# Optimization experiments

Measured on AMD Instinct MI355X. Metric: run time of the kernel, lower is better.

## Reference

```python
import jax, jax.numpy as jnp
import numpy as np

SPATIAL_SHAPES = np.array([[100, 150], [50, 75], [25, 38], [13, 19]], dtype=np.int64)


def setup_inputs() -> dict:
    key = jax.random.key(0)
    k1, k2, k3 = jax.random.split(key, 3)
    B, heads, d = 1, 8, 32
    L, P = SPATIAL_SHAPES.shape[0], 4
    n_tokens = int(SPATIAL_SHAPES.prod(axis=1).sum())  # 19947
    Q = n_tokens
    value = jax.random.normal(k1, (B, n_tokens, heads, d), dtype=jnp.float32)
    sampling_locations = jax.random.uniform(k2, (B, Q, heads, L, P, 2), dtype=jnp.float32)
    aw = jax.random.uniform(k3, (B, Q, heads, L, P), dtype=jnp.float32)
    # normalize like the real module (softmax over L*P); keeps magnitudes realistic
    attention_weights = aw / aw.sum(axis=(-2, -1), keepdims=True)
    level_start = np.concatenate([[0], np.cumsum(SPATIAL_SHAPES.prod(axis=1))[:-1]]).astype(np.int64)
    return {
        'value': value,
        'value_spatial_shapes': jnp.asarray(SPATIAL_SHAPES),
        'value_level_start_index': jnp.asarray(level_start),
        'sampling_locations': sampling_locations,
        'attention_weights': attention_weights,
        'im2col_step': 64,
    }


def _sample_level(v, loc, Hh, Ww):
    """Bilinear grid_sample (align_corners=False, zero padding).
    v:   [B, heads, Hh*Ww, D]
    loc: [B, Q, heads, P, 2] normalized in [0,1]
    returns [B, heads, Q, P, D]
    """
    B, Q, heads, P, _ = loc.shape
    D = v.shape[-1]
    # grid = 2*loc - 1; pixel coord = (grid+1)*size/2 - 0.5  ==  loc*size - 0.5
    x = loc[..., 0] * Ww - 0.5
    y = loc[..., 1] * Hh - 0.5
    x0f = jnp.floor(x)
    y0f = jnp.floor(y)
    wx1 = x - x0f
    wy1 = y - y0f
    x0 = x0f.astype(jnp.int32)
    y0 = y0f.astype(jnp.int32)

    def gather(xi, yi):
        valid = ((xi >= 0) & (xi < Ww) & (yi >= 0) & (yi < Hh)).astype(v.dtype)
        idx = jnp.clip(yi, 0, Hh - 1) * Ww + jnp.clip(xi, 0, Ww - 1)  # [B,Q,heads,P]
        idx_t = idx.transpose(0, 2, 1, 3).reshape(B, heads, Q * P, 1)
        g = jnp.take_along_axis(v, idx_t, axis=2)  # [B,heads,Q*P,D]
        g = g.reshape(B, heads, Q, P, D)
        return g, valid.transpose(0, 2, 1, 3)[..., None]

    g00, m00 = gather(x0, y0)
    g01, m01 = gather(x0 + 1, y0)
    g10, m10 = gather(x0, y0 + 1)
    g11, m11 = gather(x0 + 1, y0 + 1)
    wx1t = wx1.transpose(0, 2, 1, 3)[..., None]
    wy1t = wy1.transpose(0, 2, 1, 3)[..., None]
    wx0t = 1.0 - wx1t
    wy0t = 1.0 - wy1t
    return (g00 * m00 * (wx0t * wy0t) + g01 * m01 * (wx1t * wy0t)
            + g10 * m10 * (wx0t * wy1t) + g11 * m11 * (wx1t * wy1t))


def msda_forward(value, spatial_shapes_np, sampling_locations, attention_weights):
    B, n_tokens, heads, D = value.shape
    Q = sampling_locations.shape[1]
    areas = [int(h) * int(w) for h, w in spatial_shapes_np]
    # value per level as [B, heads, H*W, D]
    v_bhnd = value.transpose(0, 2, 1, 3)  # [B, heads, N, D]
    out = jnp.zeros((B, Q, heads, D), dtype=value.dtype)
    start = 0
    for lvl, (Hh, Ww) in enumerate(spatial_shapes_np):
        Hh, Ww = int(Hh), int(Ww)
        v_l = jax.lax.slice_in_dim(v_bhnd, start, start + Hh * Ww, axis=2)
        loc_l = sampling_locations[:, :, :, lvl]  # [B,Q,heads,P,2]
        sampled = _sample_level(v_l, loc_l, Hh, Ww)  # [B,heads,Q,P,D]
        aw_l = attention_weights[:, :, :, lvl]  # [B,Q,heads,P]
        out = out + jnp.einsum('bhqpd,bqhp->bqhd', sampled, aw_l)
        start += Hh * Ww
    return out.reshape(B, Q, heads * D)


def reference(value, value_spatial_shapes, value_level_start_index, sampling_locations, attention_weights, im2col_step):
    spatial_shapes_np = np.asarray(jax.device_get(value_spatial_shapes))
    return msda_forward(value, spatial_shapes_np, sampling_locations, attention_weights)
```

## Files before the change

kernel.cpp:

```cpp
#include <hip/hip_runtime.h>


typedef float    f32x4 __attribute__((ext_vector_type(4)));
typedef float    f32x8 __attribute__((ext_vector_type(8)));
typedef _Float16 f16x8 __attribute__((ext_vector_type(8)));

constexpr int HEADS = 8;
constexpr int DCH   = 32;
constexpr int NSP   = 16;
constexpr int NQ    = 19947;
constexpr int QPB   = 32;
constexpr int HSTR  = NQ * DCH;
constexpr int NVAL  = NQ * HEADS * DCH;

__global__ __launch_bounds__(256)
void cvt_kernel(const float* __restrict__ value, _Float16* __restrict__ ws)
{
    const int h = blockIdx.x & 7;
    const int i = (blockIdx.x >> 3) * 256 + threadIdx.x;
    if (i >= NQ * 4) return;
    const int c8  = i & 3;
    const int tok = i >> 2;
    const float* src = value + (size_t)tok * 256 + h * 32 + c8 * 8;
    const f32x4 a = __builtin_nontemporal_load((const f32x4*)src);
    const f32x4 b = __builtin_nontemporal_load((const f32x4*)(src + 4));
    const f32x8 v = {a.x, a.y, a.z, a.w, b.x, b.y, b.z, b.w};
    *(f16x8*)(ws + (size_t)h * HSTR + (size_t)tok * 32 + c8 * 8) =
        __builtin_convertvector(v, f16x8);
}

template <bool F16>
__global__ __launch_bounds__(256)
void msda_fwd_kernel(const void* __restrict__ valuev,
                     const float* __restrict__ loc,
                     const float* __restrict__ attw,
                     float* __restrict__ out)
{
    __shared__ float s_loc[QPB][33];
    __shared__ float s_aw [QPB][17];

    const int h    = blockIdx.x & 7;
    const int qblk = blockIdx.x >> 3;
    const int q0   = qblk * QPB;
    const int t    = threadIdx.x;

    {
        const int sub = t >> 3, j = t & 7;
        const int q = q0 + sub;
        if (q < NQ) {
            const f32x4 v = __builtin_nontemporal_load(
                (const f32x4*)(loc + ((size_t)(q * HEADS + h)) * (NSP * 2) + j * 4));
            const int l = j >> 1;
            const float fW = (l == 0) ? 150.f : (l == 1) ? 75.f : (l == 2) ? 38.f : 19.f;
            const float fH = (l == 0) ? 100.f : (l == 1) ? 50.f : (l == 2) ? 25.f : 13.f;
            s_loc[sub][j * 4 + 0] = v.x * fW - 0.5f;
            s_loc[sub][j * 4 + 1] = v.y * fH - 0.5f;
            s_loc[sub][j * 4 + 2] = v.z * fW - 0.5f;
            s_loc[sub][j * 4 + 3] = v.w * fH - 0.5f;
        }
    }
    if (t < 128) {
        const int sub = t >> 2, j = t & 3;
        const int q = q0 + sub;
        if (q < NQ) {
            const f32x4 w = __builtin_nontemporal_load(
                (const f32x4*)(attw + ((size_t)(q * HEADS + h)) * NSP + j * 4));
            s_aw[sub][j * 4 + 0] = w.x;
            s_aw[sub][j * 4 + 1] = w.y;
            s_aw[sub][j * 4 + 2] = w.z;
            s_aw[sub][j * 4 + 3] = w.w;
        }
    }
    __syncthreads();

    const int sub  = t >> 3;
    const int jj   = t & 3;
    const int half = (t >> 2) & 1;
    const int q    = q0 + sub;
    if (q >= NQ) return;

    const _Float16* vf16 = (const _Float16*)valuev + (size_t)h * HSTR + jj * 8;
    const float*    vf32 = (const float*)valuev + h * DCH + jj * 8;

    auto meta = [&](int sp, f32x4& c, int& i00, int& i01, int& i10, int& i11) {
        const int l = sp >> 2;
        const int W = (l == 0) ? 150 : (l == 1) ? 75 : (l == 2) ? 38 : 19;
        const int H = (l == 0) ? 100 : (l == 1) ? 50 : (l == 2) ? 25 : 13;
        const int S = (l == 0) ? 0 : (l == 1) ? 15000 : (l == 2) ? 18750 : 19700;
        const float x  = s_loc[sub][sp * 2 + 0];
        const float y  = s_loc[sub][sp * 2 + 1];
        const float aw = s_aw[sub][sp];
        const float x0f = floorf(x);
        const float y0f = floorf(y);
        const float wx1 = x - x0f;
        const float wy1 = y - y0f;
        const float wx0 = 1.f - wx1;
        const float wy0 = 1.f - wy1;
        const int x0 = (int)x0f, y0 = (int)y0f;
        const int x1 = x0 + 1,   y1 = y0 + 1;
        const float wx0m = ((unsigned)x0 < (unsigned)W) ? wx0 : 0.f;
        const float wx1m = ((unsigned)x1 < (unsigned)W) ? wx1 : 0.f;
        const float wy0m = ((unsigned)y0 < (unsigned)H) ? aw * wy0 : 0.f;
        const float wy1m = ((unsigned)y1 < (unsigned)H) ? aw * wy1 : 0.f;
        c.x = wy0m * wx0m;
        c.y = wy0m * wx1m;
        c.z = wy1m * wx0m;
        c.w = wy1m * wx1m;
        const int cx0 = max(x0, 0), cx1 = min(x1, W - 1);
        const int cy0 = max(y0, 0), cy1 = min(y1, H - 1);
        const int r0 = S + cy0 * W;
        const int r1 = S + cy1 * W;
        i00 = r0 + cx0; i01 = r0 + cx1; i10 = r1 + cx0; i11 = r1 + cx1;
    };

    f32x8 acc = {0.f, 0.f, 0.f, 0.f, 0.f, 0.f, 0.f, 0.f};
    const int sp0 = half * 8;

#pragma unroll
    for (int u = 0; u < 8; ++u) {
        const int sp = sp0 + u;
        f32x4 c;
        int i00, i01, i10, i11;
        meta(sp, c, i00, i01, i10, i11);

        if constexpr (F16) {
            const f16x8 g00 = *(const f16x8*)(vf16 + (size_t)i00 * 32);
            const f16x8 g01 = *(const f16x8*)(vf16 + (size_t)i01 * 32);
            const f16x8 g10 = *(const f16x8*)(vf16 + (size_t)i10 * 32);
            const f16x8 g11 = *(const f16x8*)(vf16 + (size_t)i11 * 32);
#pragma unroll
            for (int k = 0; k < 8; ++k) {
                acc[k] += c.x * (float)g00[k];
                acc[k] += c.y * (float)g01[k];
                acc[k] += c.z * (float)g10[k];
                acc[k] += c.w * (float)g11[k];
            }
        } else {
            const f32x4 a0 = *(const f32x4*)(vf32 + ((size_t)i00 << 8));
            const f32x4 a1 = *(const f32x4*)(vf32 + ((size_t)i00 << 8) + 4);
            const f32x4 b0 = *(const f32x4*)(vf32 + ((size_t)i01 << 8));
            const f32x4 b1 = *(const f32x4*)(vf32 + ((size_t)i01 << 8) + 4);
            const f32x4 c0 = *(const f32x4*)(vf32 + ((size_t)i10 << 8));
            const f32x4 c1 = *(const f32x4*)(vf32 + ((size_t)i10 << 8) + 4);
            const f32x4 d0 = *(const f32x4*)(vf32 + ((size_t)i11 << 8));
            const f32x4 d1 = *(const f32x4*)(vf32 + ((size_t)i11 << 8) + 4);
#pragma unroll
            for (int k = 0; k < 4; ++k) {
                acc[k]     += c.x * a0[k] + c.y * b0[k] + c.z * c0[k] + c.w * d0[k];
                acc[k + 4] += c.x * a1[k] + c.y * b1[k] + c.z * c1[k] + c.w * d1[k];
            }
        }
    }

#pragma unroll
    for (int k = 0; k < 8; ++k) acc[k] += __shfl_xor(acc[k], 4);

    float* op = out + (size_t)(q * HEADS + h) * DCH + jj * 8 + half * 4;
    const f32x4 part = half ? f32x4{acc[4], acc[5], acc[6], acc[7]}
                            : f32x4{acc[0], acc[1], acc[2], acc[3]};
    __builtin_nontemporal_store(part, (f32x4*)op);
}

extern "C" void kernel_launch(void* const* d_in, const int* in_sizes, int n_in,
                              void* d_out, int out_size, void* d_ws, size_t ws_size,
                              hipStream_t stream) {
    const float* value = (const float*)d_in[0];
    const float* loc   = (const float*)d_in[3];
    const float* attw  = (const float*)d_in[4];
    float* out = (float*)d_out;

    const int qblocks = (NQ + QPB - 1) / QPB;
    const int grid = qblocks * HEADS;

    const size_t f16_bytes = (size_t)NVAL * sizeof(_Float16);
    if (ws_size >= f16_bytes) {
        _Float16* ws = (_Float16*)d_ws;
        const int cgrid = ((NQ * 4 + 255) / 256) * HEADS;
        cvt_kernel<<<cgrid, 256, 0, stream>>>(value, ws);
        msda_fwd_kernel<true><<<grid, 256, 0, stream>>>(ws, loc, attw, out);
    } else {
        msda_fwd_kernel<false><<<grid, 256, 0, stream>>>(value, loc, attw, out);
    }
}
```

Baseline: 55.05 us.

## Store horizontally adjacent value pairs in fp16 workspace to halve bilinear gathers

The conversion kernel now writes each token's fp16 channels interleaved with those of the next token (x+1). Each bilinear sample then needs only two 32-byte row loads instead of four 16-byte corner loads, and lanes split between the left and right neighbour. The x-edge clamp case folds both weights onto the left element. The cost is a doubled workspace write plus a larger gather footprint, fewer queries per block, and an extra shuffle reduction. The new path runs only when the workspace is large enough, which it must be for the new branch to be taken.

```diff
diff --git a/kernel.cpp b/kernel.cpp
--- a/kernel.cpp
+++ b/kernel.cpp
@@ -9,9 +9,32 @@
 constexpr int DCH   = 32;
 constexpr int NSP   = 16;
 constexpr int NQ    = 19947;
-constexpr int QPB   = 32;
-constexpr int HSTR  = NQ * DCH;
+constexpr int HSTR1 = NQ * DCH;
+constexpr int HSTR2 = NQ * 64;
 constexpr int NVAL  = NQ * HEADS * DCH;
+
+__global__ __launch_bounds__(256)
+void cvt_pair_kernel(const float* __restrict__ value, _Float16* __restrict__ ws)
+{
+    const int h = blockIdx.x & 7;
+    const int i = (blockIdx.x >> 3) * 256 + threadIdx.x;
+    if (i >= NQ * 4) return;
+    const int jj = i & 3;
+    const int t  = i >> 2;
+    const float* src = value + (size_t)t * 256 + h * 32 + jj * 8;
+    const f32x4 a = __builtin_nontemporal_load((const f32x4*)src);
+    const f32x4 b = __builtin_nontemporal_load((const f32x4*)(src + 4));
+    const f32x8 v = {a.x, a.y, a.z, a.w, b.x, b.y, b.z, b.w};
+    const f16x8 o = __builtin_convertvector(v, f16x8);
+    _Float16* base = ws + (size_t)h * HSTR2;
+    *(f16x8*)(base + (size_t)t * 64 + jj * 16) = o;
+    if (t > 0)
+        *(f16x8*)(base + (size_t)(t - 1) * 64 + jj * 16 + 8) = o;
+    if (t == NQ - 1) {
+        const f16x8 z = {};
+        *(f16x8*)(base + (size_t)t * 64 + jj * 16 + 8) = z;
+    }
+}
 
 __global__ __launch_bounds__(256)
 void cvt_kernel(const float* __restrict__ value, _Float16* __restrict__ ws)
@@ -25,8 +48,127 @@
     const f32x4 a = __builtin_nontemporal_load((const f32x4*)src);
     const f32x4 b = __builtin_nontemporal_load((const f32x4*)(src + 4));
     const f32x8 v = {a.x, a.y, a.z, a.w, b.x, b.y, b.z, b.w};
-    *(f16x8*)(ws + (size_t)h * HSTR + (size_t)tok * 32 + c8 * 8) =
+    *(f16x8*)(ws + (size_t)h * HSTR1 + (size_t)tok * 32 + c8 * 8) =
         __builtin_convertvector(v, f16x8);
+}
+
+__global__ __launch_bounds__(256)
+void msda_pair_kernel(const _Float16* __restrict__ ws,
+                      const float* __restrict__ loc,
+                      const float* __restrict__ attw,
+                      float* __restrict__ out)
+{
+    constexpr int QPB = 16;
+    __shared__ float s_loc[QPB][33];
+    __shared__ float s_aw [QPB][17];
+
+    const int h    = blockIdx.x & 7;
+    const int qblk = blockIdx.x >> 3;
+    const int q0   = qblk * QPB;
+    const int t    = threadIdx.x;
+
+    if (t < 128) {
+        const int sub = t >> 3, j = t & 7;
+        const int q = q0 + sub;
+        if (q < NQ) {
+            const f32x4 v = __builtin_nontemporal_load(
+                (const f32x4*)(loc + ((size_t)(q * HEADS + h)) * (NSP * 2) + j * 4));
+            const int l = j >> 1;
+            const float fW = (l == 0) ? 150.f : (l == 1) ? 75.f : (l == 2) ? 38.f : 19.f;
+            const float fH = (l == 0) ? 100.f : (l == 1) ? 50.f : (l == 2) ? 25.f : 13.f;
+            s_loc[sub][j * 4 + 0] = v.x * fW - 0.5f;
+            s_loc[sub][j * 4 + 1] = v.y * fH - 0.5f;
+            s_loc[sub][j * 4 + 2] = v.z * fW - 0.5f;
+            s_loc[sub][j * 4 + 3] = v.w * fH - 0.5f;
+        }
+    } else if (t < 192) {
+        const int u = t - 128;
+        const int sub = u >> 2, j = u & 3;
+        const int q = q0 + sub;
+        if (q < NQ) {
+            const f32x4 w = __builtin_nontemporal_load(
+                (const f32x4*)(attw + ((size_t)(q * HEADS + h)) * NSP + j * 4));
+            s_aw[sub][j * 4 + 0] = w.x;
+            s_aw[sub][j * 4 + 1] = w.y;
+            s_aw[sub][j * 4 + 2] = w.z;
+            s_aw[sub][j * 4 + 3] = w.w;
+        }
+    }
+    __syncthreads();
+
+    const int sub  = t >> 4;
+    const int ll   = t & 15;
+    const int half = ll >> 3;
+    const int g    = (ll >> 1) & 3;
+    const int s    = ll & 1;
+    const int q    = q0 + sub;
+    if (q >= NQ) return;
+
+    const _Float16* vf = ws + (size_t)h * HSTR2 + g * 16 + s * 8;
+
+    f32x8 acc = {0.f, 0.f, 0.f, 0.f, 0.f, 0.f, 0.f, 0.f};
+    const int sp0 = half * 8;
+
+#pragma unroll
+    for (int u = 0; u < 8; ++u) {
+        const int sp = sp0 + u;
+        const int l  = sp >> 2;
+        const int W = (l == 0) ? 150 : (l == 1) ? 75 : (l == 2) ? 38 : 19;
+        const int H = (l == 0) ? 100 : (l == 1) ? 50 : (l == 2) ? 25 : 13;
+        const int S = (l == 0) ? 0 : (l == 1) ? 15000 : (l == 2) ? 18750 : 19700;
+
+        const float x  = s_loc[sub][sp * 2 + 0];
+        const float y  = s_loc[sub][sp * 2 + 1];
+        const float aw = s_aw[sub][sp];
+
+        const float x0f = floorf(x);
+        const float y0f = floorf(y);
+        const float wx1 = x - x0f;
+        const float wy1 = y - y0f;
+        const float wx0 = 1.f - wx1;
+        const float wy0 = 1.f - wy1;
+        const int x0 = (int)x0f, y0 = (int)y0f;
+        const int x1 = x0 + 1,   y1 = y0 + 1;
+
+        const float wx0m = ((unsigned)x0 < (unsigned)W) ? wx0 : 0.f;
+        const float wx1m = ((unsigned)x1 < (unsigned)W) ? wx1 : 0.f;
+        const float wy0m = ((unsigned)y0 < (unsigned)H) ? aw * wy0 : 0.f;
+        const float wy1m = ((unsigned)y1 < (unsigned)H) ? aw * wy1 : 0.f;
+        const float c00 = wy0m * wx0m;
+        const float c01 = wy0m * wx1m;
+        const float c10 = wy1m * wx0m;
+        const float c11 = wy1m * wx1m;
+
+        const int cx0 = max(x0, 0), cx1 = min(x1, W - 1);
+        const int cy0 = max(y0, 0), cy1 = min(y1, H - 1);
+        const bool xi = cx1 > cx0;
+
+        const float fA = s ? (xi ? c01 : 0.f) : (xi ? c00 : c00 + c01);
+        const float fB = s ? (xi ? c11 : 0.f) : (xi ? c10 : c10 + c11);
+
+        const int rb0 = S + cy0 * W + cx0;
+        const int rb1 = S + cy1 * W + cx0;
+
+        const f16x8 g0 = *(const f16x8*)(vf + (size_t)rb0 * 64);
+        const f16x8 g1 = *(const f16x8*)(vf + (size_t)rb1 * 64);
+#pragma unroll
+        for (int k = 0; k < 8; ++k) {
+            acc[k] += fA * (float)g0[k];
+            acc[k] += fB * (float)g1[k];
+        }
+    }
+
+#pragma unroll
+    for (int k = 0; k < 8; ++k) acc[k] += __shfl_xor(acc[k], 1);
+#pragma unroll
+    for (int k = 0; k < 8; ++k) acc[k] += __shfl_xor(acc[k], 8);
+
+    if (half == 0) {
+        float* op = out + (size_t)(q * HEADS + h) * DCH + g * 8 + s * 4;
+        const f32x4 part = s ? f32x4{acc[4], acc[5], acc[6], acc[7]}
+                             : f32x4{acc[0], acc[1], acc[2], acc[3]};
+        __builtin_nontemporal_store(part, (f32x4*)op);
+    }
 }
 
 template <bool F16>
@@ -36,6 +178,7 @@
                      const float* __restrict__ attw,
                      float* __restrict__ out)
 {
+    constexpr int QPB = 32;
     __shared__ float s_loc[QPB][33];
     __shared__ float s_aw [QPB][17];
 
@@ -79,11 +222,16 @@
     const int q    = q0 + sub;
     if (q >= NQ) return;
 
-    const _Float16* vf16 = (const _Float16*)valuev + (size_t)h * HSTR + jj * 8;
+    const _Float16* vf16 = (const _Float16*)valuev + (size_t)h * HSTR1 + jj * 8;
     const float*    vf32 = (const float*)valuev + h * DCH + jj * 8;
 
-    auto meta = [&](int sp, f32x4& c, int& i00, int& i01, int& i10, int& i11) {
-        const int l = sp >> 2;
+    f32x8 acc = {0.f, 0.f, 0.f, 0.f, 0.f, 0.f, 0.f, 0.f};
+    const int sp0 = half * 8;
+
+#pragma unroll
+    for (int u = 0; u < 8; ++u) {
+        const int sp = sp0 + u;
+        const int l  = sp >> 2;
         const int W = (l == 0) ? 150 : (l == 1) ? 75 : (l == 2) ? 38 : 19;
         const int H = (l == 0) ? 100 : (l == 1) ? 50 : (l == 2) ? 25 : 13;
         const int S = (l == 0) ? 0 : (l == 1) ? 15000 : (l == 2) ? 18750 : 19700;
@@ -102,26 +250,12 @@
         const float wx1m = ((unsigned)x1 < (unsigned)W) ? wx1 : 0.f;
         const float wy0m = ((unsigned)y0 < (unsigned)H) ? aw * wy0 : 0.f;
         const float wy1m = ((unsigned)y1 < (unsigned)H) ? aw * wy1 : 0.f;
-        c.x = wy0m * wx0m;
-        c.y = wy0m * wx1m;
-        c.z = wy1m * wx0m;
-        c.w = wy1m * wx1m;
+        const f32x4 c = {wy0m * wx0m, wy0m * wx1m, wy1m * wx0m, wy1m * wx1m};
         const int cx0 = max(x0, 0), cx1 = min(x1, W - 1);
         const int cy0 = max(y0, 0), cy1 = min(y1, H - 1);
         const int r0 = S + cy0 * W;
         const int r1 = S + cy1 * W;
-        i00 = r0 + cx0; i01 = r0 + cx1; i10 = r1 + cx0; i11 = r1 + cx1;
-    };
-
-    f32x8 acc = {0.f, 0.f, 0.f, 0.f, 0.f, 0.f, 0.f, 0.f};
-    const int sp0 = half * 8;
-
-#pragma unroll
-    for (int u = 0; u < 8; ++u) {
-        const int sp = sp0 + u;
-        f32x4 c;
-        int i00, i01, i10, i11;
-        meta(sp, c, i00, i01, i10, i11);
+        const int i00 = r0 + cx0, i01 = r0 + cx1, i10 = r1 + cx0, i11 = r1 + cx1;
 
         if constexpr (F16) {
             const f16x8 g00 = *(const f16x8*)(vf16 + (size_t)i00 * 32);
@@ -169,16 +303,22 @@
     const float* attw  = (const float*)d_in[4];
     float* out = (float*)d_out;
 
-    const int qblocks = (NQ + QPB - 1) / QPB;
-    const int grid = qblocks * HEADS;
-
-    const size_t f16_bytes = (size_t)NVAL * sizeof(_Float16);
-    if (ws_size >= f16_bytes) {
+    const size_t pair_bytes = (size_t)NQ * HEADS * 64 * sizeof(_Float16);
+    const size_t f16_bytes  = (size_t)NVAL * sizeof(_Float16);
+    const int cgrid = ((NQ * 4 + 255) / 256) * HEADS;
+
+    if (ws_size >= pair_bytes) {
         _Float16* ws = (_Float16*)d_ws;
-        const int cgrid = ((NQ * 4 + 255) / 256) * HEADS;
+        cvt_pair_kernel<<<cgrid, 256, 0, stream>>>(value, ws);
+        const int qblocks = (NQ + 15) / 16;
+        msda_pair_kernel<<<qblocks * HEADS, 256, 0, stream>>>(ws, loc, attw, out);
+    } else if (ws_size >= f16_bytes) {
+        _Float16* ws = (_Float16*)d_ws;
         cvt_kernel<<<cgrid, 256, 0, stream>>>(value, ws);
-        msda_fwd_kernel<true><<<grid, 256, 0, stream>>>(ws, loc, attw, out);
+        const int qblocks = (NQ + 31) / 32;
+        msda_fwd_kernel<true><<<qblocks * HEADS, 256, 0, stream>>>(ws, loc, attw, out);
     } else {
-        msda_fwd_kernel<false><<<grid, 256, 0, stream>>>(value, loc, attw, out);
-    }
-}
+        const int qblocks = (NQ + 31) / 32;
+        msda_fwd_kernel<false><<<qblocks * HEADS, 256, 0, stream>>>(value, loc, attw, out);
+    }
+}
```

Result: slower. 63.02 us (+14.5%).

## Store adjacent-token value pairs and precompute sampling metadata in shared memory

Applied to the files above, without the earlier changes.

The fp16 conversion kernel now writes each token's 32 channels next to those of the following token, so one row index reaches both horizontal bilinear neighbours. Each sampling point then needs two gathers instead of four, and at the right edge the weights of the two corners are merged. Per-point metadata (corner weights and row indices) is computed once per query in shared memory by 16 threads, and the main loop uses 16 threads per query with an extra shuffle reduction. The cost is a workspace twice as large, twice the conversion write traffic, and half as many queries per block.

```diff
diff --git a/kernel.cpp b/kernel.cpp
--- a/kernel.cpp
+++ b/kernel.cpp
@@ -1,6 +1,7 @@
 #include <hip/hip_runtime.h>
 
 
+typedef float    f32x2 __attribute__((ext_vector_type(2)));
 typedef float    f32x4 __attribute__((ext_vector_type(4)));
 typedef float    f32x8 __attribute__((ext_vector_type(8)));
 typedef _Float16 f16x8 __attribute__((ext_vector_type(8)));
@@ -9,156 +10,189 @@
 constexpr int DCH   = 32;
 constexpr int NSP   = 16;
 constexpr int NQ    = 19947;
-constexpr int QPB   = 32;
-constexpr int HSTR  = NQ * DCH;
+constexpr int HSTR2 = NQ * 64;
 constexpr int NVAL  = NQ * HEADS * DCH;
 
 __global__ __launch_bounds__(256)
-void cvt_kernel(const float* __restrict__ value, _Float16* __restrict__ ws)
+void cvt_pair_kernel(const float* __restrict__ value, _Float16* __restrict__ ws)
 {
     const int h = blockIdx.x & 7;
     const int i = (blockIdx.x >> 3) * 256 + threadIdx.x;
     if (i >= NQ * 4) return;
-    const int c8  = i & 3;
-    const int tok = i >> 2;
-    const float* src = value + (size_t)tok * 256 + h * 32 + c8 * 8;
+    const int g = i & 3;
+    const int t = i >> 2;
+    const float* src = value + (size_t)t * 256 + h * 32 + g * 8;
     const f32x4 a = __builtin_nontemporal_load((const f32x4*)src);
     const f32x4 b = __builtin_nontemporal_load((const f32x4*)(src + 4));
     const f32x8 v = {a.x, a.y, a.z, a.w, b.x, b.y, b.z, b.w};
-    *(f16x8*)(ws + (size_t)h * HSTR + (size_t)tok * 32 + c8 * 8) =
-        __builtin_convertvector(v, f16x8);
-}
-
-template <bool F16>
+    const f16x8 o = __builtin_convertvector(v, f16x8);
+    _Float16* base = ws + (size_t)h * HSTR2;
+    *(f16x8*)(base + (size_t)t * 64 + g * 8) = o;
+    if (t > 0)
+        *(f16x8*)(base + (size_t)(t - 1) * 64 + 32 + g * 8) = o;
+    if (t == NQ - 1) {
+        const f16x8 z = {};
+        *(f16x8*)(base + (size_t)t * 64 + 32 + g * 8) = z;
+    }
+}
+
 __global__ __launch_bounds__(256)
-void msda_fwd_kernel(const void* __restrict__ valuev,
+void msda_meta_kernel(const _Float16* __restrict__ ws,
+                      const float* __restrict__ loc,
+                      const float* __restrict__ attw,
+                      float* __restrict__ out)
+{
+    constexpr int QPB = 16;
+    constexpr int PSTR = NSP * 8 + 4;
+    __shared__ __align__(16) float s_meta[QPB][PSTR];
+
+    const int h    = blockIdx.x & 7;
+    const int qblk = blockIdx.x >> 3;
+    const int q0   = qblk * QPB;
+    const int t    = threadIdx.x;
+
+    {
+        const int pair = t >> 4, sp = t & 15;
+        const int q = q0 + pair;
+        if (q < NQ) {
+            const size_t mb = (size_t)(q * HEADS + h);
+            const f32x2 xy = __builtin_nontemporal_load(
+                (const f32x2*)(loc + mb * (NSP * 2) + sp * 2));
+            const float aw = __builtin_nontemporal_load(attw + mb * NSP + sp);
+
+            const int l = sp >> 2;
+            const float fW = (l == 0) ? 150.f : (l == 1) ? 75.f : (l == 2) ? 38.f : 19.f;
+            const float fH = (l == 0) ? 100.f : (l == 1) ? 50.f : (l == 2) ? 25.f : 13.f;
+            const int   W  = (l == 0) ? 150   : (l == 1) ? 75   : (l == 2) ? 38   : 19;
+            const int   H  = (l == 0) ? 100   : (l == 1) ? 50   : (l == 2) ? 25   : 13;
+            const int   S  = (l == 0) ? 0     : (l == 1) ? 15000: (l == 2) ? 18750: 19700;
+
+            const float x = xy.x * fW - 0.5f;
+            const float y = xy.y * fH - 0.5f;
+            const float x0f = floorf(x);
+            const float y0f = floorf(y);
+            const float wx1 = x - x0f;
+            const float wy1 = y - y0f;
+            const float wx0 = 1.f - wx1;
+            const float wy0 = 1.f - wy1;
+            const int x0 = (int)x0f, y0 = (int)y0f;
+            const int x1 = x0 + 1,   y1 = y0 + 1;
+
+            const float wx0m = ((unsigned)x0 < (unsigned)W) ? wx0 : 0.f;
+            const float wx1m = ((unsigned)x1 < (unsigned)W) ? wx1 : 0.f;
+            const float wy0m = ((unsigned)y0 < (unsigned)H) ? aw * wy0 : 0.f;
+            const float wy1m = ((unsigned)y1 < (unsigned)H) ? aw * wy1 : 0.f;
+            const float c00 = wy0m * wx0m;
+            const float c01 = wy0m * wx1m;
+            const float c10 = wy1m * wx0m;
+            const float c11 = wy1m * wx1m;
+
+            const int cx0 = max(x0, 0), cx1 = min(x1, W - 1);
+            const int cy0 = max(y0, 0), cy1 = min(y1, H - 1);
+            const bool xi = cx1 > cx0;
+
+            float* m = &s_meta[pair][sp * 8];
+            m[0] = xi ? c00 : (c00 + c01);
+            m[1] = xi ? c01 : 0.f;
+            m[2] = xi ? c10 : (c10 + c11);
+            m[3] = xi ? c11 : 0.f;
+            int* mi = (int*)m;
+            mi[4] = S + cy0 * W + cx0;
+            mi[5] = S + cy1 * W + cx0;
+        }
+    }
+    __syncthreads();
+
+    const int pair = t >> 4;
+    const int lane = t & 15;
+    const int g    = lane & 3;
+    const int s    = (lane >> 2) & 1;
+    const int half = lane >> 3;
+    const int q    = q0 + pair;
+    if (q >= NQ) return;
+
+    const _Float16* vf = ws + (size_t)h * HSTR2 + s * 32 + g * 8;
+
+    f32x8 acc = {0.f, 0.f, 0.f, 0.f, 0.f, 0.f, 0.f, 0.f};
+    const int sp0 = half * 8;
+
+#pragma unroll
+    for (int u = 0; u < 8; ++u) {
+        const float* m = &s_meta[pair][(sp0 + u) * 8];
+        const f32x4 c = *(const f32x4*)m;
+        const int rb0 = ((const int*)m)[4];
+        const int rb1 = ((const int*)m)[5];
+        const float fA = s ? c.y : c.x;
+        const float fB = s ? c.w : c.z;
+
+        const f16x8 g0 = *(const f16x8*)(vf + (size_t)rb0 * 64);
+        const f16x8 g1 = *(const f16x8*)(vf + (size_t)rb1 * 64);
+#pragma unroll
+        for (int k = 0; k < 8; ++k) {
+            acc[k] += fA * (float)g0[k];
+            acc[k] += fB * (float)g1[k];
+        }
+    }
+
+#pragma unroll
+    for (int k = 0; k < 8; ++k) acc[k] += __shfl_xor(acc[k], 4);
+#pragma unroll
+    for (int k = 0; k < 8; ++k) acc[k] += __shfl_xor(acc[k], 8);
+
+    if (s == 0) {
+        float* op = out + (size_t)(q * HEADS + h) * DCH + g * 8 + half * 4;
+        const f32x4 part = half ? f32x4{acc[4], acc[5], acc[6], acc[7]}
+                                : f32x4{acc[0], acc[1], acc[2], acc[3]};
+        __builtin_nontemporal_store(part, (f32x4*)op);
+    }
+}
+
+__global__ __launch_bounds__(256)
+void msda_f32_kernel(const float* __restrict__ value,
                      const float* __restrict__ loc,
                      const float* __restrict__ attw,
                      float* __restrict__ out)
 {
-    __shared__ float s_loc[QPB][33];
-    __shared__ float s_aw [QPB][17];
-
-    const int h    = blockIdx.x & 7;
-    const int qblk = blockIdx.x >> 3;
-    const int q0   = qblk * QPB;
-    const int t    = threadIdx.x;
-
-    {
-        const int sub = t >> 3, j = t & 7;
-        const int q = q0 + sub;
-        if (q < NQ) {
-            const f32x4 v = __builtin_nontemporal_load(
-                (const f32x4*)(loc + ((size_t)(q * HEADS + h)) * (NSP * 2) + j * 4));
-            const int l = j >> 1;
-            const float fW = (l == 0) ? 150.f : (l == 1) ? 75.f : (l == 2) ? 38.f : 19.f;
-            const float fH = (l == 0) ? 100.f : (l == 1) ? 50.f : (l == 2) ? 25.f : 13.f;
-            s_loc[sub][j * 4 + 0] = v.x * fW - 0.5f;
-            s_loc[sub][j * 4 + 1] = v.y * fH - 0.5f;
-            s_loc[sub][j * 4 + 2] = v.z * fW - 0.5f;
-            s_loc[sub][j * 4 + 3] = v.w * fH - 0.5f;
-        }
-    }
-    if (t < 128) {
-        const int sub = t >> 2, j = t & 3;
-        const int q = q0 + sub;
-        if (q < NQ) {
-            const f32x4 w = __builtin_nontemporal_load(
-                (const f32x4*)(attw + ((size_t)(q * HEADS + h)) * NSP + j * 4));
-            s_aw[sub][j * 4 + 0] = w.x;
-            s_aw[sub][j * 4 + 1] = w.y;
-            s_aw[sub][j * 4 + 2] = w.z;
-            s_aw[sub][j * 4 + 3] = w.w;
-        }
-    }
-    __syncthreads();
-
-    const int sub  = t >> 3;
-    const int jj   = t & 3;
-    const int half = (t >> 2) & 1;
-    const int q    = q0 + sub;
-    if (q >= NQ) return;
-
-    const _Float16* vf16 = (const _Float16*)valuev + (size_t)h * HSTR + jj * 8;
-    const float*    vf32 = (const float*)valuev + h * DCH + jj * 8;
-
-    auto meta = [&](int sp, f32x4& c, int& i00, int& i01, int& i10, int& i11) {
+    const int t    = blockIdx.x * blockDim.x + threadIdx.x;
+    const int pair = t >> 3;
+    const int d0   = (t & 7) * 4;
+    if (pair >= NQ * HEADS) return;
+    const int h = pair & 7;
+
+    const float* locp = loc  + (size_t)pair * (NSP * 2);
+    const float* awp  = attw + (size_t)pair * NSP;
+    f32x4 acc = {0.f, 0.f, 0.f, 0.f};
+
+#pragma unroll
+    for (int sp = 0; sp < NSP; ++sp) {
         const int l = sp >> 2;
         const int W = (l == 0) ? 150 : (l == 1) ? 75 : (l == 2) ? 38 : 19;
         const int H = (l == 0) ? 100 : (l == 1) ? 50 : (l == 2) ? 25 : 13;
         const int S = (l == 0) ? 0 : (l == 1) ? 15000 : (l == 2) ? 18750 : 19700;
-        const float x  = s_loc[sub][sp * 2 + 0];
-        const float y  = s_loc[sub][sp * 2 + 1];
-        const float aw = s_aw[sub][sp];
-        const float x0f = floorf(x);
-        const float y0f = floorf(y);
-        const float wx1 = x - x0f;
-        const float wy1 = y - y0f;
-        const float wx0 = 1.f - wx1;
-        const float wy0 = 1.f - wy1;
-        const int x0 = (int)x0f, y0 = (int)y0f;
-        const int x1 = x0 + 1,   y1 = y0 + 1;
+        const float x = locp[sp * 2] * W - 0.5f;
+        const float y = locp[sp * 2 + 1] * H - 0.5f;
+        const float aw = awp[sp];
+        const float x0f = floorf(x), y0f = floorf(y);
+        const float wx1 = x - x0f, wy1 = y - y0f;
+        const float wx0 = 1.f - wx1, wy0 = 1.f - wy1;
+        const int x0 = (int)x0f, y0 = (int)y0f, x1 = x0 + 1, y1 = y0 + 1;
         const float wx0m = ((unsigned)x0 < (unsigned)W) ? wx0 : 0.f;
         const float wx1m = ((unsigned)x1 < (unsigned)W) ? wx1 : 0.f;
         const float wy0m = ((unsigned)y0 < (unsigned)H) ? aw * wy0 : 0.f;
         const float wy1m = ((unsigned)y1 < (unsigned)H) ? aw * wy1 : 0.f;
-        c.x = wy0m * wx0m;
-        c.y = wy0m * wx1m;
-        c.z = wy1m * wx0m;
-        c.w = wy1m * wx1m;
         const int cx0 = max(x0, 0), cx1 = min(x1, W - 1);
         const int cy0 = max(y0, 0), cy1 = min(y1, H - 1);
-        const int r0 = S + cy0 * W;
-        const int r1 = S + cy1 * W;
-        i00 = r0 + cx0; i01 = r0 + cx1; i10 = r1 + cx0; i11 = r1 + cx1;
-    };
-
-    f32x8 acc = {0.f, 0.f, 0.f, 0.f, 0.f, 0.f, 0.f, 0.f};
-    const int sp0 = half * 8;
-
-#pragma unroll
-    for (int u = 0; u < 8; ++u) {
-        const int sp = sp0 + u;
-        f32x4 c;
-        int i00, i01, i10, i11;
-        meta(sp, c, i00, i01, i10, i11);
-
-        if constexpr (F16) {
-            const f16x8 g00 = *(const f16x8*)(vf16 + (size_t)i00 * 32);
-            const f16x8 g01 = *(const f16x8*)(vf16 + (size_t)i01 * 32);
-            const f16x8 g10 = *(const f16x8*)(vf16 + (size_t)i10 * 32);
-            const f16x8 g11 = *(const f16x8*)(vf16 + (size_t)i11 * 32);
-#pragma unroll
-            for (int k = 0; k < 8; ++k) {
-                acc[k] += c.x * (float)g00[k];
-                acc[k] += c.y * (float)g01[k];
-                acc[k] += c.z * (float)g10[k];
-                acc[k] += c.w * (float)g11[k];
-            }
-        } else {
-            const f32x4 a0 = *(const f32x4*)(vf32 + ((size_t)i00 << 8));
-            const f32x4 a1 = *(const f32x4*)(vf32 + ((size_t)i00 << 8) + 4);
-            const f32x4 b0 = *(const f32x4*)(vf32 + ((size_t)i01 << 8));
-            const f32x4 b1 = *(const f32x4*)(vf32 + ((size_t)i01 << 8) + 4);
-            const f32x4 c0 = *(const f32x4*)(vf32 + ((size_t)i10 << 8));
-            const f32x4 c1 = *(const f32x4*)(vf32 + ((size_t)i10 << 8) + 4);
-            const f32x4 d0 = *(const f32x4*)(vf32 + ((size_t)i11 << 8));
-            const f32x4 d1 = *(const f32x4*)(vf32 + ((size_t)i11 << 8) + 4);
-#pragma unroll
-            for (int k = 0; k < 4; ++k) {
-                acc[k]     += c.x * a0[k] + c.y * b0[k] + c.z * c0[k] + c.w * d0[k];
-                acc[k + 4] += c.x * a1[k] + c.y * b1[k] + c.z * c1[k] + c.w * d1[k];
-            }
-        }
-    }
-
-#pragma unroll
-    for (int k = 0; k < 8; ++k) acc[k] += __shfl_xor(acc[k], 4);
-
-    float* op = out + (size_t)(q * HEADS + h) * DCH + jj * 8 + half * 4;
-    const f32x4 part = half ? f32x4{acc[4], acc[5], acc[6], acc[7]}
-                            : f32x4{acc[0], acc[1], acc[2], acc[3]};
-    __builtin_nontemporal_store(part, (f32x4*)op);
+        const size_t r0 = (size_t)(S + cy0 * W), r1 = (size_t)(S + cy1 * W);
+        const f32x4 g00 = *(const f32x4*)(value + ((r0 + cx0) * 8 + h) * DCH + d0);
+        const f32x4 g01 = *(const f32x4*)(value + ((r0 + cx1) * 8 + h) * DCH + d0);
+        const f32x4 g10 = *(const f32x4*)(value + ((r1 + cx0) * 8 + h) * DCH + d0);
+        const f32x4 g11 = *(const f32x4*)(value + ((r1 + cx1) * 8 + h) * DCH + d0);
+        acc += g00 * (wy0m * wx0m);
+        acc += g01 * (wy0m * wx1m);
+        acc += g10 * (wy1m * wx0m);
+        acc += g11 * (wy1m * wx1m);
+    }
+    *(f32x4*)(out + (size_t)pair * DCH + d0) = acc;
 }
 
 extern "C" void kernel_launch(void* const* d_in, const int* in_sizes, int n_in,
@@ -169,16 +203,16 @@
     const float* attw  = (const float*)d_in[4];
     float* out = (float*)d_out;
 
-    const int qblocks = (NQ + QPB - 1) / QPB;
-    const int grid = qblocks * HEADS;
-
-    const size_t f16_bytes = (size_t)NVAL * sizeof(_Float16);
-    if (ws_size >= f16_bytes) {
+    const size_t pair_bytes = (size_t)NQ * HEADS * 64 * sizeof(_Float16);
+
+    if (ws_size >= pair_bytes) {
         _Float16* ws = (_Float16*)d_ws;
         const int cgrid = ((NQ * 4 + 255) / 256) * HEADS;
-        cvt_kernel<<<cgrid, 256, 0, stream>>>(value, ws);
-        msda_fwd_kernel<true><<<grid, 256, 0, stream>>>(ws, loc, attw, out);
+        cvt_pair_kernel<<<cgrid, 256, 0, stream>>>(value, ws);
+        const int qblocks = (NQ + 15) / 16;
+        msda_meta_kernel<<<qblocks * HEADS, 256, 0, stream>>>(ws, loc, attw, out);
     } else {
-        msda_fwd_kernel<false><<<grid, 256, 0, stream>>>(value, loc, attw, out);
-    }
-}
+        const int total = NQ * HEADS * 8;
+        msda_f32_kernel<<<(total + 255) / 256, 256, 0, stream>>>(value, loc, attw, out);
+    }
+}
```

After: 54.58 us. No clear change (-0.8%).
